# Optimization experiments

Hardware: AMD Instinct MI355X
Metric: run time of the kernel (lower is better)

## Reference

```python
import jax, jax.numpy as jnp
import numpy as np

E, T, C = 100000, 1000000, 64


def setup_inputs() -> dict:
    key = jax.random.key(0)
    k1, k2, k3, k4, k5 = jax.random.split(key, 5)
    xij = jax.random.normal(k1, (E, C), dtype=jnp.float32)
    r = jax.random.normal(k2, (E, 3), dtype=jnp.float32)
    attn = jax.random.normal(k3, (1, C), dtype=jnp.float32)
    t_src = jax.random.randint(k4, (T,), 0, E)
    t_dst = jax.random.randint(k5, (T,), 0, E)
    return {"xij": xij, "r": r, "attn": attn, "t_src": t_src, "t_dst": t_dst}


def reference(xij, r, attn, t_src, t_dst):
    n_edges, channels = xij.shape
    # unit bond directions (negated, as in the torch code)
    rnorm = -r / jnp.linalg.norm(r, axis=1, keepdims=True)          # [E, 3]
    # triplet angle cosines via gather + dot (fn.u_dot_v)
    cos_jik = jnp.sum(rnorm[t_src] * rnorm[t_dst], axis=-1)         # [T]
    # Chebyshev angular expansion: T_n(x) = cos(n * arccos(x)), n = 0..C-1
    theta = jnp.arccos(jnp.clip(cos_jik, -1.0 + 1e-6, 1.0 - 1e-6))  # [T]
    z_jik = jnp.cos(theta[:, None] * jnp.arange(channels, dtype=theta.dtype)[None, :])  # [T, C]
    # fn.u_add_v on bond features
    x_jik = xij[t_src] + xij[t_dst]                                 # [T, C]
    e_jik = jax.nn.silu(z_jik + x_jik)                              # [T, C]
    a = jnp.sum(e_jik * attn, axis=-1)                              # [T]
    # edge_softmax over incoming triplets of each destination bond
    a_max = jax.ops.segment_max(a, t_dst, num_segments=n_edges)     # [E]
    ex = jnp.exp(a - a_max[t_dst])                                  # [T]
    denom = jax.ops.segment_sum(ex, t_dst, num_segments=n_edges)    # [E]
    alpha = ex / denom[t_dst]                                       # [T]
    # gather-multiply-scatter-sum aggregation (u_mul_e + sum)
    m = xij[t_src] * alpha[:, None]                                 # [T, C]
    ft = jax.ops.segment_sum(m, t_dst, num_segments=n_edges)        # [E, C]
    return ft
```

## Files before the change

kernel.cpp:

```cpp
#include <hip/hip_runtime.h>
#include <math.h>


#define LOG2E 1.4426950408889634f
#define SCAN_B 256

__global__ void ta_init(const float* __restrict__ r,
                        float4* __restrict__ rnorm4,
                        int E) {
    int i = blockIdx.x * blockDim.x + threadIdx.x;
    if (i < E) {
        float rx = r[i * 3 + 0], ry = r[i * 3 + 1], rz = r[i * 3 + 2];
        float inv = rsqrtf(rx * rx + ry * ry + rz * rz);
        rnorm4[i] = make_float4(rx * inv, ry * inv, rz * inv, 0.f);
    }
}

__global__ void ta_hist(const int* __restrict__ t_dst,
                        int* __restrict__ rowptr, int T) {
    int t = blockIdx.x * blockDim.x + threadIdx.x;
    if (t < T) atomicAdd(&rowptr[t_dst[t]], 1);
}

__global__ void ta_scan1(int* __restrict__ rowptr, int* __restrict__ bsum, int E) {
    __shared__ int sm[SCAN_B];
    int i = blockIdx.x * SCAN_B + threadIdx.x;
    int v = (i < E) ? rowptr[i] : 0;
    sm[threadIdx.x] = v;
    __syncthreads();
    int x = v;
    for (int o = 1; o < SCAN_B; o <<= 1) {
        int y = (threadIdx.x >= (unsigned)o) ? sm[threadIdx.x - o] : 0;
        __syncthreads();
        x += y;
        sm[threadIdx.x] = x;
        __syncthreads();
    }
    if (i < E) rowptr[i] = x - v;
    if (threadIdx.x == SCAN_B - 1) bsum[blockIdx.x] = x;
}

__global__ void ta_scan2(int* __restrict__ bsum, int n) {
    __shared__ int sm[512];
    int tid = threadIdx.x;
    int v = (tid < n) ? bsum[tid] : 0;
    sm[tid] = v;
    __syncthreads();
    int x = v;
    for (int o = 1; o < 512; o <<= 1) {
        int y = (tid >= o) ? sm[tid - o] : 0;
        __syncthreads();
        x += y;
        sm[tid] = x;
        __syncthreads();
    }
    if (tid < n) bsum[tid] = x - v;
}

__global__ void ta_scan3(int* __restrict__ rowptr, const int* __restrict__ bsum, int E) {
    int i = blockIdx.x * blockDim.x + threadIdx.x;
    if (i < E) rowptr[i] += bsum[i >> 8];
}

__global__ void ta_scatter(const int* __restrict__ t_dst,
                           const int* __restrict__ t_src,
                           int* __restrict__ rowptr,
                           int* __restrict__ ssorted, int T) {
    int t = blockIdx.x * blockDim.x + threadIdx.x;
    if (t < T) {
        int pos = atomicAdd(&rowptr[t_dst[t]], 1);
        ssorted[pos] = t_src[t];
    }
}

__global__ void ta_fused(const float* __restrict__ xij,
                         const float* __restrict__ attn,
                         const float4* __restrict__ rnorm4,
                         const int* __restrict__ ssorted,
                         const int* __restrict__ segend,
                         float* __restrict__ ft, int E) {
    const int lane = threadIdx.x & 63;
    const int waveId = blockIdx.x * (blockDim.x >> 6) + (threadIdx.x >> 6);
    if (waveId >= E) return;
    const int e = waveId;
    const int g   = lane >> 3;
    const int sub = lane & 7;
    const int c0  = sub * 8;
    const float fc0 = (float)c0;

    int end = segend[e];
    int start = (e == 0) ? 0 : segend[e - 1];
    int len = end - start;

    float xd[8], at[8];
    const float* xdp = xij + (size_t)e * 64 + c0;
    *(float4*)&xd[0] = *(const float4*)(xdp);
    *(float4*)&xd[4] = *(const float4*)(xdp + 4);
    *(float4*)&at[0] = *(const float4*)(attn + c0);
    *(float4*)&at[4] = *(const float4*)(attn + c0 + 4);
    const float4 rd = rnorm4[e];

    float m = -3.402823466e38f, den = 0.f;
    float acc[8] = {0, 0, 0, 0, 0, 0, 0, 0};

    for (int chunk = start; chunk < end; chunk += 64) {
        int cl = end - chunk; if (cl > 64) cl = 64;
        int idx = chunk + lane; if (idx >= end) idx = end - 1;
        int sv = ssorted[idx];
        float4 rs = rnorm4[sv];
        float cosj = rs.x * rd.x + rs.y * rd.y + rs.z * rd.z;
        cosj = fminf(fmaxf(cosj, -1.0f + 1e-6f), 1.0f - 1e-6f);
        float th2p = acosf(cosj) * 0.15915493667125702f;

        for (int j8 = 0; j8 < cl; j8 += 8) {
            int jj = j8 + g;
            bool active = (jj < cl);
            int jc = active ? jj : 0;
            float th = __shfl(th2p, jc, 64);
            float tc = __shfl(cosj, jc, 64);
            int   s  = __shfl(sv,   jc, 64);

            const float* xsp = xij + (size_t)s * 64 + c0;
            float xs[8];
            *(float4*)&xs[0] = *(const float4*)(xsp);
            *(float4*)&xs[4] = *(const float4*)(xsp + 4);

            float r0 = th * fc0;
            float z0 = __builtin_amdgcn_cosf(r0 - floorf(r0));
            float r1 = r0 + th;
            float z1 = __builtin_amdgcn_cosf(r1 - floorf(r1));
            float twoc = 2.0f * tc;

            float part = 0.f;
            float zkm1 = z0, zk = z1;
            #pragma unroll
            for (int k = 0; k < 8; ++k) {
                float z = (k == 0) ? z0 : zk;
                float v = z + xs[k] + xd[k];
                float ez = __builtin_amdgcn_exp2f(-v * LOG2E);
                float sl = v * __builtin_amdgcn_rcpf(1.0f + ez);
                part = fmaf(sl, at[k], part);
                if (k > 0) {
                    float zn = fmaf(twoc, zk, -zkm1);
                    zkm1 = zk; zk = zn;
                }
            }
            part += __shfl_xor(part, 1, 64);
            part += __shfl_xor(part, 2, 64);
            part += __shfl_xor(part, 4, 64);
            float contrib = active ? part : -3.402823466e38f;
            float mn = fmaxf(m, contrib);
            float scale = __builtin_amdgcn_exp2f((m - mn) * LOG2E);
            float p     = __builtin_amdgcn_exp2f((contrib - mn) * LOG2E);
            den = den * scale + p;
            #pragma unroll
            for (int k = 0; k < 8; ++k) acc[k] = fmaf(p, xs[k], acc[k] * scale);
            m = mn;
        }
    }

    if (len > 1) {
        #pragma unroll
        for (int off = 8; off < 64; off <<= 1) {
            float m2 = __shfl_xor(m, off, 64);
            float d2 = __shfl_xor(den, off, 64);
            float mn = fmaxf(m, m2);
            float s1 = __builtin_amdgcn_exp2f((m - mn) * LOG2E);
            float s2 = __builtin_amdgcn_exp2f((m2 - mn) * LOG2E);
            den = den * s1 + d2 * s2;
            #pragma unroll
            for (int k = 0; k < 8; ++k) {
                float a2 = __shfl_xor(acc[k], off, 64);
                acc[k] = acc[k] * s1 + a2 * s2;
            }
            m = mn;
        }
    }

    float rden = (len > 0) ? __builtin_amdgcn_rcpf(den) : 0.f;
    if (lane < 8) {
        float out[8];
        #pragma unroll
        for (int k = 0; k < 8; ++k) out[k] = acc[k] * rden;
        float* fo = ft + (size_t)e * 64 + lane * 8;
        *(float4*)(fo)     = *(float4*)&out[0];
        *(float4*)(fo + 4) = *(float4*)&out[4];
    }
}

extern "C" void kernel_launch(void* const* d_in, const int* in_sizes, int n_in,
                              void* d_out, int out_size, void* d_ws, size_t ws_size,
                              hipStream_t stream) {
    const float* xij   = (const float*)d_in[0];
    const float* r     = (const float*)d_in[1];
    const float* attn  = (const float*)d_in[2];
    const int*   t_src = (const int*)d_in[3];
    const int*   t_dst = (const int*)d_in[4];
    float* ft = (float*)d_out;

    const int E = in_sizes[1] / 3;
    const int T = in_sizes[3];

    char* ws = (char*)d_ws;
    float4* rnorm4  = (float4*)ws;
    int*    ssorted = (int*)(ws + (size_t)E * 16);
    int*    rowptr  = (int*)((char*)ssorted + (size_t)T * 4);
    int*    bsum    = (int*)((char*)rowptr + (size_t)E * 4);

    const int nScanBlocks = (E + SCAN_B - 1) / SCAN_B;

    hipMemsetAsync(rowptr, 0, (size_t)E * 4, stream);
    ta_init<<<(E + 255) / 256, 256, 0, stream>>>(r, rnorm4, E);
    ta_hist<<<(T + 255) / 256, 256, 0, stream>>>(t_dst, rowptr, T);
    ta_scan1<<<nScanBlocks, SCAN_B, 0, stream>>>(rowptr, bsum, E);
    ta_scan2<<<1, 512, 0, stream>>>(bsum, nScanBlocks);
    ta_scan3<<<nScanBlocks, SCAN_B, 0, stream>>>(rowptr, bsum, E);
    ta_scatter<<<(T + 255) / 256, 256, 0, stream>>>(t_dst, t_src, rowptr, ssorted, T);
    ta_fused<<<(E + 3) / 4, 256, 0, stream>>>(xij, attn, rnorm4, ssorted, rowptr, ft, E);
}
```

Before: 267.7 us.

## Merge CSR build stages into one cooperative kernel with grid syncs

```diff
diff --git a/kernel.cpp b/kernel.cpp
--- a/kernel.cpp
+++ b/kernel.cpp
@@ -1,75 +1,110 @@
 #include <hip/hip_runtime.h>
+#include <hip/hip_cooperative_groups.h>
 #include <math.h>
+
+namespace cg = cooperative_groups;
 
 
 #define LOG2E 1.4426950408889634f
 #define SCAN_B 256
-
-__global__ void ta_init(const float* __restrict__ r,
-                        float4* __restrict__ rnorm4,
-                        int E) {
-    int i = blockIdx.x * blockDim.x + threadIdx.x;
-    if (i < E) {
+#define BUILD_BLOCKS 1024
+#define BUILD_THREADS 256
+
+__global__ void __launch_bounds__(BUILD_THREADS, 8)
+ta_build(const float* __restrict__ r,
+         const int* __restrict__ t_dst,
+         const int* __restrict__ t_src,
+         float4* __restrict__ rnorm4,
+         int* __restrict__ rowptr,
+         int* __restrict__ bsum,
+         int* __restrict__ ssorted,
+         int E, int T, int nScanBlocks) {
+    cg::grid_group grid = cg::this_grid();
+    const int tid = threadIdx.x;
+    const int gtid = blockIdx.x * BUILD_THREADS + tid;
+    const int nthreads = gridDim.x * BUILD_THREADS;
+    __shared__ int sm[512];
+
+    for (int i = gtid; i < E; i += nthreads) {
         float rx = r[i * 3 + 0], ry = r[i * 3 + 1], rz = r[i * 3 + 2];
         float inv = rsqrtf(rx * rx + ry * ry + rz * rz);
         rnorm4[i] = make_float4(rx * inv, ry * inv, rz * inv, 0.f);
-    }
-}
-
-__global__ void ta_hist(const int* __restrict__ t_dst,
-                        int* __restrict__ rowptr, int T) {
-    int t = blockIdx.x * blockDim.x + threadIdx.x;
-    if (t < T) atomicAdd(&rowptr[t_dst[t]], 1);
-}
-
-__global__ void ta_scan1(int* __restrict__ rowptr, int* __restrict__ bsum, int E) {
-    __shared__ int sm[SCAN_B];
-    int i = blockIdx.x * SCAN_B + threadIdx.x;
-    int v = (i < E) ? rowptr[i] : 0;
-    sm[threadIdx.x] = v;
-    __syncthreads();
-    int x = v;
-    for (int o = 1; o < SCAN_B; o <<= 1) {
-        int y = (threadIdx.x >= (unsigned)o) ? sm[threadIdx.x - o] : 0;
+        rowptr[i] = 0;
+    }
+    grid.sync();
+
+    {
+        const int T4 = T >> 2;
+        const int4* td4 = (const int4*)t_dst;
+        for (int i = gtid; i < T4; i += nthreads) {
+            int4 d = td4[i];
+            atomicAdd(&rowptr[d.x], 1);
+            atomicAdd(&rowptr[d.y], 1);
+            atomicAdd(&rowptr[d.z], 1);
+            atomicAdd(&rowptr[d.w], 1);
+        }
+        for (int t = (T4 << 2) + gtid; t < T; t += nthreads)
+            atomicAdd(&rowptr[t_dst[t]], 1);
+    }
+    grid.sync();
+
+    if (blockIdx.x < (unsigned)nScanBlocks) {
+        int i = blockIdx.x * SCAN_B + tid;
+        int v = (i < E) ? rowptr[i] : 0;
+        sm[tid] = v;
         __syncthreads();
-        x += y;
-        sm[threadIdx.x] = x;
+        int x = v;
+        for (int o = 1; o < SCAN_B; o <<= 1) {
+            int y = (tid >= o) ? sm[tid - o] : 0;
+            __syncthreads();
+            x += y;
+            sm[tid] = x;
+            __syncthreads();
+        }
+        if (i < E) rowptr[i] = x - v;
+        if (tid == SCAN_B - 1) bsum[blockIdx.x] = x;
+    }
+    grid.sync();
+
+    if (blockIdx.x == 0) {
+        int i0 = 2 * tid, i1 = 2 * tid + 1;
+        int v0 = (i0 < nScanBlocks) ? bsum[i0] : 0;
+        int v1 = (i1 < nScanBlocks) ? bsum[i1] : 0;
+        int pair = v0 + v1;
+        sm[tid] = pair;
         __syncthreads();
-    }
-    if (i < E) rowptr[i] = x - v;
-    if (threadIdx.x == SCAN_B - 1) bsum[blockIdx.x] = x;
-}
-
-__global__ void ta_scan2(int* __restrict__ bsum, int n) {
-    __shared__ int sm[512];
-    int tid = threadIdx.x;
-    int v = (tid < n) ? bsum[tid] : 0;
-    sm[tid] = v;
-    __syncthreads();
-    int x = v;
-    for (int o = 1; o < 512; o <<= 1) {
-        int y = (tid >= o) ? sm[tid - o] : 0;
-        __syncthreads();
-        x += y;
-        sm[tid] = x;
-        __syncthreads();
-    }
-    if (tid < n) bsum[tid] = x - v;
-}
-
-__global__ void ta_scan3(int* __restrict__ rowptr, const int* __restrict__ bsum, int E) {
-    int i = blockIdx.x * blockDim.x + threadIdx.x;
-    if (i < E) rowptr[i] += bsum[i >> 8];
-}
-
-__global__ void ta_scatter(const int* __restrict__ t_dst,
-                           const int* __restrict__ t_src,
-                           int* __restrict__ rowptr,
-                           int* __restrict__ ssorted, int T) {
-    int t = blockIdx.x * blockDim.x + threadIdx.x;
-    if (t < T) {
-        int pos = atomicAdd(&rowptr[t_dst[t]], 1);
-        ssorted[pos] = t_src[t];
+        int x = pair;
+        for (int o = 1; o < 256; o <<= 1) {
+            int y = (tid >= o) ? sm[tid - o] : 0;
+            __syncthreads();
+            x += y;
+            sm[tid] = x;
+            __syncthreads();
+        }
+        int excl = x - pair;
+        if (i0 < nScanBlocks) bsum[i0] = excl;
+        if (i1 < nScanBlocks) bsum[i1] = excl + v0;
+    }
+    grid.sync();
+
+    for (int i = gtid; i < E; i += nthreads)
+        rowptr[i] += bsum[i >> 8];
+    grid.sync();
+
+    {
+        const int T4 = T >> 2;
+        const int4* td4 = (const int4*)t_dst;
+        const int4* ts4 = (const int4*)t_src;
+        for (int i = gtid; i < T4; i += nthreads) {
+            int4 d = td4[i];
+            int4 s = ts4[i];
+            ssorted[atomicAdd(&rowptr[d.x], 1)] = s.x;
+            ssorted[atomicAdd(&rowptr[d.y], 1)] = s.y;
+            ssorted[atomicAdd(&rowptr[d.z], 1)] = s.z;
+            ssorted[atomicAdd(&rowptr[d.w], 1)] = s.w;
+        }
+        for (int t = (T4 << 2) + gtid; t < T; t += nthreads)
+            ssorted[atomicAdd(&rowptr[t_dst[t]], 1)] = t_src[t];
     }
 }
 
@@ -198,8 +233,8 @@
     const int*   t_dst = (const int*)d_in[4];
     float* ft = (float*)d_out;
 
-    const int E = in_sizes[1] / 3;
-    const int T = in_sizes[3];
+    int E = in_sizes[1] / 3;
+    int T = in_sizes[3];
 
     char* ws = (char*)d_ws;
     float4* rnorm4  = (float4*)ws;
@@ -207,14 +242,17 @@
     int*    rowptr  = (int*)((char*)ssorted + (size_t)T * 4);
     int*    bsum    = (int*)((char*)rowptr + (size_t)E * 4);
 
-    const int nScanBlocks = (E + SCAN_B - 1) / SCAN_B;
-
-    hipMemsetAsync(rowptr, 0, (size_t)E * 4, stream);
-    ta_init<<<(E + 255) / 256, 256, 0, stream>>>(r, rnorm4, E);
-    ta_hist<<<(T + 255) / 256, 256, 0, stream>>>(t_dst, rowptr, T);
-    ta_scan1<<<nScanBlocks, SCAN_B, 0, stream>>>(rowptr, bsum, E);
-    ta_scan2<<<1, 512, 0, stream>>>(bsum, nScanBlocks);
-    ta_scan3<<<nScanBlocks, SCAN_B, 0, stream>>>(rowptr, bsum, E);
-    ta_scatter<<<(T + 255) / 256, 256, 0, stream>>>(t_dst, t_src, rowptr, ssorted, T);
+    int nScanBlocks = (E + SCAN_B - 1) / SCAN_B;
+
+    const float* r_arg = r;
+    const int* td_arg = t_dst;
+    const int* ts_arg = t_src;
+    void* args[] = {(void*)&r_arg, (void*)&td_arg, (void*)&ts_arg,
+                    (void*)&rnorm4, (void*)&rowptr, (void*)&bsum,
+                    (void*)&ssorted, (void*)&E, (void*)&T, (void*)&nScanBlocks};
+    hipLaunchCooperativeKernel((const void*)ta_build,
+                               dim3(BUILD_BLOCKS), dim3(BUILD_THREADS),
+                               args, 0, stream);
+
     ta_fused<<<(E + 3) / 4, 256, 0, stream>>>(xij, attn, rnorm4, ssorted, rowptr, ft, E);
 }
```

Result: slower. 733.5 us (+174.0%).
